# Performance work log

Hardware: AMD Instinct MI355X
Metric: run time of the kernel (lower is better)

The kernel has to match this reference:

```python
import jax, jax.numpy as jnp
import numpy as np

N = 100000      # nodes
E = 1600000     # edges (before self-loops)
DIN = 256
D = 128         # dmid == dout
L = 4           # n_layers
ALPHA = 0.5
THETA = 1.0
EPS = 1e-5      # pyg LayerNorm default eps


def setup_inputs() -> dict:
    key = jax.random.key(0)
    ks = jax.random.split(key, 6)
    x = jax.random.normal(ks[0], (N, DIN), jnp.float32)
    edge_index = jax.random.randint(ks[1], (2, E), 0, N)
    lin1_w = jax.random.normal(ks[2], (D, DIN), jnp.float32) * (1.0 / np.sqrt(DIN))
    lin1_b = jnp.zeros((D,), jnp.float32)
    w1 = jax.random.normal(ks[3], (L, D, D), jnp.float32) * (1.0 / np.sqrt(D))
    w2 = jax.random.normal(ks[4], (L, D, D), jnp.float32) * (1.0 / np.sqrt(D))
    norm_w = jnp.ones((D,), jnp.float32)
    norm_b = jnp.zeros((D,), jnp.float32)
    return {"x": x, "edge_index": edge_index, "lin1_w": lin1_w, "lin1_b": lin1_b,
            "w1": w1, "w2": w2, "norm_w": norm_w, "norm_b": norm_b}


def reference(x, edge_index, lin1_w, lin1_b, w1, w2, norm_w, norm_b):
    # --- gcn_norm: add self-loops, symmetric degree normalization ---
    sl = jnp.arange(N)
    row = jnp.concatenate([edge_index[0], sl])  # sources
    col = jnp.concatenate([edge_index[1], sl])  # targets (aggregation index)
    deg = jax.ops.segment_sum(jnp.ones(row.shape[0], jnp.float32), col, num_segments=N)
    dis = jax.lax.rsqrt(deg)  # deg >= 1 thanks to self-loops
    enorm = dis[row] * dis[col]  # [E+N]

    # --- f_0 = relu(lin1(x)); prev_h = 0 so x_0 arg == f_0 ---
    f0 = jax.nn.relu(x @ lin1_w.T + lin1_b)  # [N, D]
    x0 = ALPHA * f0
    f = f0

    for i in range(L):
        beta = float(np.log(THETA / (i + 1) + 1.0))
        # sparse neighbor aggregation: h = A_hat @ f
        h = jax.ops.segment_sum(f[row] * enorm[:, None], col, num_segments=N)
        h = h * (1.0 - ALPHA)
        # shared_weights=False: two separate identity/weight mixes
        out = ((1.0 - beta) * h + beta * (h @ w1[i])
               + (1.0 - beta) * x0 + beta * (x0 @ w2[i]))
        # pyg LayerNorm mode='graph', batch=None: normalize over all nodes+channels
        m = out.mean()
        s = jnp.sqrt(jnp.mean((out - m) ** 2))
        out = (out - m) / (s + EPS) * norm_w + norm_b
        f = jax.nn.relu(out)

    # dmid == dout -> lin2 is Identity
    return jax.nn.relu(f)
```

## Files before the change

kernel.cpp:

```cpp
#include <hip/hip_runtime.h>
#include <math.h>

constexpr int N    = 100000;
constexpr int E    = 1600000;
constexpr int DIN  = 256;
constexpr int D    = 128;
constexpr int L    = 4;
constexpr float EPS = 1e-5f;
constexpr int NBIN = 256;
constexpr int BINW = 391;
constexpr int SLOT = 8192;

typedef __attribute__((ext_vector_type(8))) short bf16x8;
typedef __attribute__((ext_vector_type(4))) float f32x4;
typedef __attribute__((ext_vector_type(2))) float f32x2;

__device__ inline ushort f2b(float f) {
    uint u = __float_as_uint(f);
    uint r = u + 0x7fffu + ((u >> 16) & 1u);
    return (ushort)(r >> 16);
}
__device__ inline float b2f(ushort b) { return __uint_as_float(((uint)b) << 16); }


__global__ __launch_bounds__(256) void k_countbin(const int* __restrict__ row,
        const int* __restrict__ col, int* __restrict__ cnt, int* __restrict__ bfill,
        int2* __restrict__ stag) {
    __shared__ int hist[NBIN];
    __shared__ int base[NBIN];
    int t = threadIdx.x;
    int e0 = blockIdx.x * 2048 + t * 8;
    if (t < NBIN) hist[t] = 0;
    __syncthreads();
    int r[8], c[8], li[8];
    bool v[8];
    if (e0 + 7 < E) {
        *(int4*)&c[0] = ((const int4*)(col + e0))[0];
        *(int4*)&c[4] = ((const int4*)(col + e0))[1];
        *(int4*)&r[0] = ((const int4*)(row + e0))[0];
        *(int4*)&r[4] = ((const int4*)(row + e0))[1];
        #pragma unroll
        for (int j = 0; j < 8; j++) v[j] = true;
    } else {
        #pragma unroll
        for (int j = 0; j < 8; j++) {
            v[j] = (e0 + j < E);
            if (v[j]) { c[j] = col[e0 + j]; r[j] = row[e0 + j]; }
        }
    }
    #pragma unroll
    for (int j = 0; j < 8; j++) if (v[j]) {
        atomicAdd(&cnt[c[j]], 1);
        li[j] = atomicAdd(&hist[c[j] / BINW], 1);
    }
    __syncthreads();
    if (t < NBIN) base[t] = hist[t] ? atomicAdd(&bfill[t], hist[t]) : 0;
    __syncthreads();
    #pragma unroll
    for (int j = 0; j < 8; j++) if (v[j]) {
        int b = c[j] / BINW;
        stag[(size_t)b * SLOT + base[b] + li[j]] = make_int2(r[j], c[j]);
    }
}

__global__ void k_sumdis(const int* __restrict__ cnt, int* __restrict__ bsum,
                         float* __restrict__ dis) {
    __shared__ int s[256];
    int base = blockIdx.x * 1024;
    int t = threadIdx.x;
    int a = 0;
    for (int j = 0; j < 4; j++) {
        int idx = base + t * 4 + j;
        if (idx < N) {
            int cv = cnt[idx];
            a += cv;
            dis[idx] = rsqrtf((float)cv + 1.0f);
        }
    }
    s[t] = a; __syncthreads();
    for (int off = 128; off > 0; off >>= 1) {
        if (t < off) s[t] += s[t + off];
        __syncthreads();
    }
    if (t == 0) bsum[blockIdx.x] = s[0];
}

__global__ void k_scan(int* __restrict__ bsum, int nb) {
    __shared__ int s[128];
    int t = threadIdx.x;
    int v = (t < nb) ? bsum[t] : 0;
    s[t] = v; __syncthreads();
    for (int off = 1; off < 128; off <<= 1) {
        int x = (t >= off) ? s[t - off] : 0;
        __syncthreads();
        s[t] += x;
        __syncthreads();
    }
    if (t < nb) bsum[t] = s[t] - v;
}

__global__ void k_offsets(const int* __restrict__ cnt, const int* __restrict__ bsum,
                          int* __restrict__ offs, int* __restrict__ cur) {
    __shared__ int ls[256];
    int b = blockIdx.x, t = threadIdx.x;
    int base = b * 1024;
    int v[4]; int s = 0;
    for (int j = 0; j < 4; j++) {
        int idx = base + t * 4 + j;
        v[j] = (idx < N) ? cnt[idx] : 0;
        s += v[j];
    }
    ls[t] = s; __syncthreads();
    for (int off = 1; off < 256; off <<= 1) {
        int x = (t >= off) ? ls[t - off] : 0;
        __syncthreads();
        ls[t] += x;
        __syncthreads();
    }
    int excl = ((t == 0) ? 0 : ls[t - 1]) + bsum[b];
    for (int j = 0; j < 4; j++) {
        int idx = base + t * 4 + j;
        if (idx < N) { offs[idx] = excl; cur[idx] = excl; }
        excl += v[j];
        if (idx == N - 1) offs[N] = excl;
    }
}

__global__ __launch_bounds__(256) void k_unbin(const int2* __restrict__ stag,
        const int* __restrict__ bfill, const float* __restrict__ dis,
        int* __restrict__ cur, int2* __restrict__ csr) {
    int b = blockIdx.x & (NBIN - 1);
    int part = blockIdx.x >> 8;
    int n = bfill[b];
    const int2* sbase = stag + (size_t)b * SLOT;
    for (int i = part * 256 + threadIdx.x; i < n; i += 1024) {
        int2 rc = sbase[i];
        float v = dis[rc.x] * dis[rc.y];
        int pos = atomicAdd(&cur[rc.y], 1);
        csr[pos] = make_int2(rc.x, __float_as_int(v));
    }
}


__global__ void k_prep_w(const float* __restrict__ lin1_w, const float* __restrict__ w1,
                         const float* __restrict__ w2, float4 betas,
                         ushort* __restrict__ wb0, ushort* __restrict__ wbc) {
    int i = blockIdx.x * 256 + threadIdx.x;
    if (i < D * DIN) wb0[i] = f2b(lin1_w[i]);
    if (i < L * D * 256) {
        int l = i >> 15, r = i & 32767, d = r >> 8, k = r & 255;
        float beta = (l == 0) ? betas.x : (l == 1) ? betas.y : (l == 2) ? betas.z : betas.w;
        float v;
        if (k < 128) v = beta * w1[l * 16384 + k * 128 + d] + ((k == d) ? (1.f - beta) : 0.f);
        else { int kk = k - 128; v = beta * w2[l * 16384 + kk * 128 + d] + ((kk == d) ? (1.f - beta) : 0.f); }
        wbc[l * 32768 + d * 256 + k] = f2b(v);
    }
}


__global__ __launch_bounds__(512, 2) void k_f0_mfma(const float* __restrict__ x,
        const ushort* __restrict__ wb, const float* __restrict__ bias,
        ushort* __restrict__ f_bf, ushort* __restrict__ x0_bf) {
    __shared__ uint4 Bl[4096];
    int t = threadIdx.x;
    #pragma unroll
    for (int it = 0; it < 8; it++) {
        int d = it * 512 + t, c = d >> 5, ck = d & 31;
        Bl[c * 32 + (ck ^ (c & 7))] = ((const uint4*)wb)[d];
    }
    __syncthreads();

    int wv = t >> 6, lane = t & 63;
    int l16 = lane & 15, g16 = lane >> 4;
    int row0 = (blockIdx.x * 8 + wv) * 16;
    if (row0 >= N) return;

    const uint4* xb = (const uint4*)(x + (size_t)(row0 + l16) * 256);
    uint4 xr[16];
    #pragma unroll
    for (int ks = 0; ks < 8; ks++) {
        xr[2 * ks]     = xb[ks * 8 + g16 * 2];
        xr[2 * ks + 1] = xb[ks * 8 + g16 * 2 + 1];
    }

    f32x4 acc[8];
    #pragma unroll
    for (int n = 0; n < 8; n++) acc[n] = f32x4{0.f, 0.f, 0.f, 0.f};

    #pragma unroll
    for (int ks = 0; ks < 8; ks++) {
        float4 lo = *(const float4*)&xr[2 * ks];
        float4 hi = *(const float4*)&xr[2 * ks + 1];
        uint4 p;
        p.x = (uint)f2b(lo.x) | ((uint)f2b(lo.y) << 16);
        p.y = (uint)f2b(lo.z) | ((uint)f2b(lo.w) << 16);
        p.z = (uint)f2b(hi.x) | ((uint)f2b(hi.y) << 16);
        p.w = (uint)f2b(hi.z) | ((uint)f2b(hi.w) << 16);
        bf16x8 a = *(bf16x8*)&p;
        int xo = (ks * 4 + g16) ^ (l16 & 7);
        const char* bp = (const char*)Bl + l16 * 512 + xo * 16;
        #pragma unroll
        for (int n = 0; n < 8; n++) {
            bf16x8 b = *(const bf16x8*)(bp + n * 8192);
            acc[n] = __builtin_amdgcn_mfma_f32_16x16x32_bf16(a, b, acc[n], 0, 0, 0);
        }
    }

    float bc[8];
    #pragma unroll
    for (int n = 0; n < 8; n++) bc[n] = bias[n * 16 + l16];
    #pragma unroll
    for (int j = 0; j < 4; j++) {
        int gr = row0 + g16 * 4 + j;
        #pragma unroll
        for (int n = 0; n < 8; n++) {
            float r = fmaxf(acc[n][j] + bc[n], 0.f);
            size_t o = (size_t)gr * 128 + n * 16 + l16;
            f_bf[o] = f2b(r);
            x0_bf[o] = f2b(0.5f * r);
        }
    }
}


__global__ __launch_bounds__(512, 2) void k_combine_mfma(const ushort* __restrict__ g_bf,
        const ushort* __restrict__ x0_bf, const ushort* __restrict__ wb,
        ushort* __restrict__ h_bf, float* __restrict__ sr) {
    __shared__ uint4 Bl[4096];
    __shared__ float red1[512];
    __shared__ float red2[512];
    int t = threadIdx.x;
    #pragma unroll
    for (int it = 0; it < 8; it++) {
        int d = it * 512 + t, c = d >> 5, ck = d & 31;
        Bl[c * 32 + (ck ^ (c & 7))] = ((const uint4*)wb)[d];
    }
    __syncthreads();

    int wv = t >> 6, lane = t & 63;
    int l16 = lane & 15, g16 = lane >> 4;
    int row0 = (blockIdx.x * 8 + wv) * 16;
    bool active = row0 < N;

    f32x4 acc[8];
    #pragma unroll
    for (int n = 0; n < 8; n++) acc[n] = f32x4{0.f, 0.f, 0.f, 0.f};

    if (active) {
        const uint4* ga = (const uint4*)(g_bf  + (size_t)(row0 + l16) * 128);
        const uint4* xa = (const uint4*)(x0_bf + (size_t)(row0 + l16) * 128);
        uint4 ar[8];
        #pragma unroll
        for (int ks = 0; ks < 4; ks++) ar[ks]     = ga[ks * 4 + g16];
        #pragma unroll
        for (int ks = 0; ks < 4; ks++) ar[ks + 4] = xa[ks * 4 + g16];

        #pragma unroll
        for (int ks = 0; ks < 8; ks++) {
            bf16x8 a = *(bf16x8*)&ar[ks];
            int xo = (ks * 4 + g16) ^ (l16 & 7);
            const char* bp = (const char*)Bl + l16 * 512 + xo * 16;
            #pragma unroll
            for (int n = 0; n < 8; n++) {
                bf16x8 b = *(const bf16x8*)(bp + n * 8192);
                acc[n] = __builtin_amdgcn_mfma_f32_16x16x32_bf16(a, b, acc[n], 0, 0, 0);
            }
        }
    }

    float sum = 0.f, sq = 0.f;
    if (active) {
        #pragma unroll
        for (int n = 0; n < 8; n++)
            #pragma unroll
            for (int j = 0; j < 4; j++) { float v = acc[n][j]; sum += v; sq += v * v; }
        #pragma unroll
        for (int j = 0; j < 4; j++) {
            int gr = row0 + g16 * 4 + j;
            #pragma unroll
            for (int n = 0; n < 8; n++)
                h_bf[(size_t)gr * 128 + n * 16 + l16] = f2b(acc[n][j]);
        }
    }

    red1[t] = sum; red2[t] = sq; __syncthreads();
    for (int off = 256; off > 0; off >>= 1) {
        if (t < off) { red1[t] += red1[t + off]; red2[t] += red2[t + off]; }
        __syncthreads();
    }
    if (t == 0) { atomicAdd(&sr[0], red1[0]); atomicAdd(&sr[1], red2[0]); }
}


template <int AFFINE>
__global__ __launch_bounds__(256) void k_agg(const ushort* __restrict__ src,
        const int* __restrict__ offs, const int2* __restrict__ csr,
        const float* __restrict__ dis, const float* __restrict__ sr,
        const float* __restrict__ nw, const float* __restrict__ nb,
        ushort* __restrict__ g_bf) {
    int node = blockIdx.x * 4 + (threadIdx.x >> 6);
    if (node >= N) return;
    int lane = threadIdx.x & 63;
    int q = lane >> 4, cl = lane & 15;
    const uint4* fu = (const uint4*)src;

    f32x2 sc[4], sh[4];
    if constexpr (AFFINE) {
        const float inv_n = 1.0f / ((float)N * (float)D);
        float m = sr[0] * inv_n;
        float var = fmaxf(sr[1] * inv_n - m * m, 0.f);
        float inv = 1.0f / (sqrtf(var) + EPS);
        #pragma unroll
        for (int p = 0; p < 4; p++) {
            float w0 = nw[cl * 8 + 2 * p], w1 = nw[cl * 8 + 2 * p + 1];
            sc[p] = f32x2{inv * w0, inv * w1};
            sh[p] = f32x2{nb[cl * 8 + 2 * p]     - m * inv * w0,
                          nb[cl * 8 + 2 * p + 1] - m * inv * w1};
        }
    }

    f32x2 a2[4];
    #pragma unroll
    for (int p = 0; p < 4; p++) a2[p] = f32x2{0.f, 0.f};

    auto acc8 = [&](float val, uint4 rv) {
        uint uu[4] = {rv.x, rv.y, rv.z, rv.w};
        f32x2 v2 = {val, val};
        #pragma unroll
        for (int p = 0; p < 4; p++) {
            f32x2 c;
            c.x = __uint_as_float(uu[p] << 16);
            c.y = __uint_as_float(uu[p] & 0xffff0000u);
            if constexpr (AFFINE) {
                c = __builtin_elementwise_fma(c, sc[p], sh[p]);
                c = __builtin_elementwise_max(c, f32x2{0.f, 0.f});
            }
            a2[p] = __builtin_elementwise_fma(v2, c, a2[p]);
        }
    };

    float dv = dis[node];
    acc8((q == 0) ? dv * dv : 0.f, fu[(size_t)node * 16 + cl]);

    int end = offs[node + 1];
    int i = offs[node] + q * 4;
    if (i < end) {
        int2 rA[4], rB[4];
        uint4 wA[4];
        #pragma unroll
        for (int s = 0; s < 4; s++) rA[s] = csr[min(i + s, end - 1)];
        #pragma unroll
        for (int s = 0; s < 4; s++) wA[s] = fu[(size_t)rA[s].x * 16 + cl];
        #pragma unroll
        for (int s = 0; s < 4; s++) rB[s] = csr[min(i + 16 + s, end - 1)];
        while (i + 16 < end) {
            uint4 wB[4];
            #pragma unroll
            for (int s = 0; s < 4; s++) wB[s] = fu[(size_t)rB[s].x * 16 + cl];
            int2 rC[4];
            #pragma unroll
            for (int s = 0; s < 4; s++) rC[s] = csr[min(i + 32 + s, end - 1)];
            #pragma unroll
            for (int s = 0; s < 4; s++) acc8(__int_as_float(rA[s].y), wA[s]);
            #pragma unroll
            for (int s = 0; s < 4; s++) { rA[s] = rB[s]; wA[s] = wB[s]; rB[s] = rC[s]; }
            i += 16;
        }
        #pragma unroll
        for (int s = 0; s < 4; s++) {
            float v = (i + s < end) ? __int_as_float(rA[s].y) : 0.f;
            acc8(v, wA[s]);
        }
    }

    #pragma unroll
    for (int p = 0; p < 4; p++) {
        a2[p].x += __shfl_xor(a2[p].x, 16, 64);
        a2[p].x += __shfl_xor(a2[p].x, 32, 64);
        a2[p].y += __shfl_xor(a2[p].y, 16, 64);
        a2[p].y += __shfl_xor(a2[p].y, 32, 64);
    }
    if (q == 0) {
        uint4 o;
        o.x = (uint)f2b(0.5f * a2[0].x) | ((uint)f2b(0.5f * a2[0].y) << 16);
        o.y = (uint)f2b(0.5f * a2[1].x) | ((uint)f2b(0.5f * a2[1].y) << 16);
        o.z = (uint)f2b(0.5f * a2[2].x) | ((uint)f2b(0.5f * a2[2].y) << 16);
        o.w = (uint)f2b(0.5f * a2[3].x) | ((uint)f2b(0.5f * a2[3].y) << 16);
        ((uint4*)g_bf)[(size_t)node * 16 + cl] = o;
    }
}


__global__ void k_ln_final(const ushort* __restrict__ ob, const float* __restrict__ sr,
                           const float* __restrict__ nw, const float* __restrict__ nb,
                           float* __restrict__ fout) {
    int i = blockIdx.x * 256 + threadIdx.x;
    if (i >= N * 16) return;
    const float inv_n = 1.0f / ((float)N * (float)D);
    float m = sr[0] * inv_n;
    float var = fmaxf(sr[1] * inv_n - m * m, 0.f);
    float inv = 1.0f / (sqrtf(var) + EPS);
    uint4 v = ((const uint4*)ob)[i];
    int c = (i & 15) * 8;
    uint vv[4] = {v.x, v.y, v.z, v.w};
    float r[8];
    #pragma unroll
    for (int qd = 0; qd < 4; qd++) {
        float lo = b2f((ushort)(vv[qd] & 0xffff));
        float hi = b2f((ushort)(vv[qd] >> 16));
        r[2 * qd]     = fmaxf((lo - m) * inv * nw[c + 2 * qd]     + nb[c + 2 * qd], 0.f);
        r[2 * qd + 1] = fmaxf((hi - m) * inv * nw[c + 2 * qd + 1] + nb[c + 2 * qd + 1], 0.f);
    }
    float4 o0 = {r[0], r[1], r[2], r[3]};
    float4 o1 = {r[4], r[5], r[6], r[7]};
    ((float4*)fout)[2 * i] = o0;
    ((float4*)fout)[2 * i + 1] = o1;
}


extern "C" void kernel_launch(void* const* d_in, const int* in_sizes, int n_in,
                              void* d_out, int out_size, void* d_ws, size_t ws_size,
                              hipStream_t stream) {
    const float* x      = (const float*)d_in[0];
    const int*   ei     = (const int*)d_in[1];
    const float* lin1_w = (const float*)d_in[2];
    const float* lin1_b = (const float*)d_in[3];
    const float* w1     = (const float*)d_in[4];
    const float* w2     = (const float*)d_in[5];
    const float* nw     = (const float*)d_in[6];
    const float* nb     = (const float*)d_in[7];
    const int* row = ei;
    const int* col = ei + E;
    float* fout = (float*)d_out;

    char* ws = (char*)d_ws;
    size_t off0 = 0;
    auto alloc = [&](size_t bytes) -> char* {
        char* p = ws + off0;
        off0 = (off0 + bytes + 255) & ~(size_t)255;
        return p;
    };
    ushort* f_bf    = (ushort*)alloc((size_t)N * D * 2);
    ushort* x0_bf   = (ushort*)alloc((size_t)N * D * 2);
    ushort* g_bf    = (ushort*)alloc((size_t)N * D * 2);
    ushort* h_bf    = (ushort*)alloc((size_t)N * D * 2);
    float*  dis     = (float*) alloc((size_t)N * 4);
    char*   zblk    = alloc((size_t)N * 4 + NBIN * 4 + 64);
    int*    cnt     = (int*)zblk;
    int*    bfill   = (int*)(zblk + (size_t)N * 4);
    float*  stats   = (float*)(zblk + (size_t)N * 4 + NBIN * 4);
    int*    offs    = (int*)   alloc((size_t)(N + 1) * 4);
    int*    cur     = (int*)   alloc((size_t)N * 4);
    int*    bsum    = (int*)   alloc((size_t)128 * 4);
    int2*   stag    = (int2*)  alloc((size_t)NBIN * SLOT * 8);
    int2*   csr     = (int2*)  alloc((size_t)E * 8);
    ushort* wb0     = (ushort*)alloc((size_t)D * DIN * 2);
    ushort* wbc     = (ushort*)alloc((size_t)L * D * 256 * 2);

    hipMemsetAsync(zblk, 0, (size_t)N * 4 + NBIN * 4 + 64, stream);

    k_countbin<<<(E + 2047) / 2048, 256, 0, stream>>>(row, col, cnt, bfill, stag);
    int nbk = (N + 1023) / 1024;
    k_sumdis<<<nbk, 256, 0, stream>>>(cnt, bsum, dis);
    k_scan<<<1, 128, 0, stream>>>(bsum, nbk);
    k_offsets<<<nbk, 256, 0, stream>>>(cnt, bsum, offs, cur);
    k_unbin<<<NBIN * 4, 256, 0, stream>>>(stag, bfill, dis, cur, csr);

    float4 betas;
    betas.x = logf(1.0f / 1.0f + 1.0f);
    betas.y = logf(1.0f / 2.0f + 1.0f);
    betas.z = logf(1.0f / 3.0f + 1.0f);
    betas.w = logf(1.0f / 4.0f + 1.0f);
    k_prep_w<<<(L * D * 256 + 255) / 256, 256, 0, stream>>>(lin1_w, w1, w2, betas, wb0, wbc);

    int GB = (N / 16 + 7) / 8;
    k_f0_mfma<<<GB, 512, 0, stream>>>(x, wb0, lin1_b, f_bf, x0_bf);

    int AGB = (N + 3) / 4;
    for (int i = 0; i < L; i++) {
        if (i == 0)
            k_agg<0><<<AGB, 256, 0, stream>>>(f_bf, offs, csr, dis, nullptr, nw, nb, g_bf);
        else
            k_agg<1><<<AGB, 256, 0, stream>>>(h_bf, offs, csr, dis, stats + 2 * (i - 1),
                                              nw, nb, g_bf);
        k_combine_mfma<<<GB, 512, 0, stream>>>(g_bf, x0_bf, wbc + (size_t)i * D * 256,
                                               h_bf, stats + 2 * i);
    }
    k_ln_final<<<(N * 16 + 255) / 256, 256, 0, stream>>>(h_bf, stats + 6, nw, nb, fout);
}
```

Before: 570.7 us.

## Merge f0 GEMM, edge binning and weight prep into one role-split launch

Merges three independent kernels (edge count/binning, weight preparation, and the first-layer MFMA GEMM) into a single launch whose blocks pick a role by block index. Even and odd blocks are interleaved between the GEMM and the binning, and the tail blocks convert the combined layer weights. The GEMM blocks now convert lin1_w to bf16 themselves when staging it into shared memory, so the separate wb0 buffer goes away. The aim is to cut launch overhead and let the memory-bound binning overlap with the compute-bound GEMM. In exchange, binning blocks now use 512 threads with 4 edges each and inherit the larger shared-memory and launch-bounds footprint of the GEMM role.

Result: faster. 529.3 us, median of 2 (-7.2%).

```diff
diff --git a/kernel.cpp b/kernel.cpp
--- a/kernel.cpp
+++ b/kernel.cpp
@@ -11,6 +11,10 @@
 constexpr int BINW = 391;
 constexpr int SLOT = 8192;
 
+constexpr int F0B   = 782;
+constexpr int CBB   = 782;
+constexpr int PREPB = 64;
+
 typedef __attribute__((ext_vector_type(8))) short bf16x8;
 typedef __attribute__((ext_vector_type(4))) float f32x4;
 typedef __attribute__((ext_vector_type(2))) float f32x2;
@@ -23,45 +27,133 @@
 __device__ inline float b2f(ushort b) { return __uint_as_float(((uint)b) << 16); }
 
 
-__global__ __launch_bounds__(256) void k_countbin(const int* __restrict__ row,
-        const int* __restrict__ col, int* __restrict__ cnt, int* __restrict__ bfill,
-        int2* __restrict__ stag) {
-    __shared__ int hist[NBIN];
-    __shared__ int base[NBIN];
+__global__ __launch_bounds__(512, 2) void k_f0_countbin(
+        const float* __restrict__ x, const float* __restrict__ lin1_w,
+        const float* __restrict__ bias, ushort* __restrict__ f_bf,
+        ushort* __restrict__ x0_bf,
+        const int* __restrict__ row, const int* __restrict__ col,
+        int* __restrict__ cnt, int* __restrict__ bfill, int2* __restrict__ stag,
+        const float* __restrict__ w1, const float* __restrict__ w2, float4 betas,
+        ushort* __restrict__ wbc) {
+    __shared__ uint4 Bl[4096];
     int t = threadIdx.x;
-    int e0 = blockIdx.x * 2048 + t * 8;
-    if (t < NBIN) hist[t] = 0;
+
+    if (blockIdx.x >= F0B + CBB) {
+        int base = (blockIdx.x - (F0B + CBB)) * 2048 + t * 4;
+        #pragma unroll
+        for (int j = 0; j < 4; j++) {
+            int i = base + j;
+            if (i < L * D * 256) {
+                int l = i >> 15, r = i & 32767, d = r >> 8, k = r & 255;
+                float beta = (l == 0) ? betas.x : (l == 1) ? betas.y
+                           : (l == 2) ? betas.z : betas.w;
+                float v;
+                if (k < 128) v = beta * w1[l * 16384 + k * 128 + d] + ((k == d) ? (1.f - beta) : 0.f);
+                else { int kk = k - 128; v = beta * w2[l * 16384 + kk * 128 + d] + ((kk == d) ? (1.f - beta) : 0.f); }
+                wbc[l * 32768 + d * 256 + k] = f2b(v);
+            }
+        }
+        return;
+    }
+
+    int role = blockIdx.x & 1, rid = blockIdx.x >> 1;
+
+    if (role == 1) {
+        int* hist = (int*)Bl;
+        int* base = hist + NBIN;
+        if (t < NBIN) hist[t] = 0;
+        __syncthreads();
+        int e0 = rid * 2048 + t * 4;
+        bool val = (e0 < E);
+        int r[4], c[4], li[4];
+        if (val) {
+            *(int4*)&c[0] = *(const int4*)(col + e0);
+            *(int4*)&r[0] = *(const int4*)(row + e0);
+            #pragma unroll
+            for (int j = 0; j < 4; j++) {
+                atomicAdd(&cnt[c[j]], 1);
+                li[j] = atomicAdd(&hist[c[j] / BINW], 1);
+            }
+        }
+        __syncthreads();
+        if (t < NBIN) base[t] = hist[t] ? atomicAdd(&bfill[t], hist[t]) : 0;
+        __syncthreads();
+        if (val) {
+            #pragma unroll
+            for (int j = 0; j < 4; j++) {
+                int b = c[j] / BINW;
+                stag[(size_t)b * SLOT + base[b] + li[j]] = make_int2(r[j], c[j]);
+            }
+        }
+        return;
+    }
+
+    #pragma unroll
+    for (int it = 0; it < 8; it++) {
+        int d = it * 512 + t, c = d >> 5, ck = d & 31;
+        const float4* src = (const float4*)(lin1_w + c * 256 + ck * 8);
+        float4 lo = src[0], hi = src[1];
+        uint4 p;
+        p.x = (uint)f2b(lo.x) | ((uint)f2b(lo.y) << 16);
+        p.y = (uint)f2b(lo.z) | ((uint)f2b(lo.w) << 16);
+        p.z = (uint)f2b(hi.x) | ((uint)f2b(hi.y) << 16);
+        p.w = (uint)f2b(hi.z) | ((uint)f2b(hi.w) << 16);
+        Bl[c * 32 + (ck ^ (c & 7))] = p;
+    }
     __syncthreads();
-    int r[8], c[8], li[8];
-    bool v[8];
-    if (e0 + 7 < E) {
-        *(int4*)&c[0] = ((const int4*)(col + e0))[0];
-        *(int4*)&c[4] = ((const int4*)(col + e0))[1];
-        *(int4*)&r[0] = ((const int4*)(row + e0))[0];
-        *(int4*)&r[4] = ((const int4*)(row + e0))[1];
-        #pragma unroll
-        for (int j = 0; j < 8; j++) v[j] = true;
-    } else {
-        #pragma unroll
-        for (int j = 0; j < 8; j++) {
-            v[j] = (e0 + j < E);
-            if (v[j]) { c[j] = col[e0 + j]; r[j] = row[e0 + j]; }
-        }
-    }
-    #pragma unroll
-    for (int j = 0; j < 8; j++) if (v[j]) {
-        atomicAdd(&cnt[c[j]], 1);
-        li[j] = atomicAdd(&hist[c[j] / BINW], 1);
-    }
-    __syncthreads();
-    if (t < NBIN) base[t] = hist[t] ? atomicAdd(&bfill[t], hist[t]) : 0;
-    __syncthreads();
-    #pragma unroll
-    for (int j = 0; j < 8; j++) if (v[j]) {
-        int b = c[j] / BINW;
-        stag[(size_t)b * SLOT + base[b] + li[j]] = make_int2(r[j], c[j]);
-    }
-}
+
+    int wv = t >> 6, lane = t & 63;
+    int l16 = lane & 15, g16 = lane >> 4;
+    int row0 = (rid * 8 + wv) * 16;
+    if (row0 >= N) return;
+
+    const uint4* xb = (const uint4*)(x + (size_t)(row0 + l16) * 256);
+    uint4 xr[16];
+    #pragma unroll
+    for (int ks = 0; ks < 8; ks++) {
+        xr[2 * ks]     = xb[ks * 8 + g16 * 2];
+        xr[2 * ks + 1] = xb[ks * 8 + g16 * 2 + 1];
+    }
+
+    f32x4 acc[8];
+    #pragma unroll
+    for (int n = 0; n < 8; n++) acc[n] = f32x4{0.f, 0.f, 0.f, 0.f};
+
+    #pragma unroll
+    for (int ks = 0; ks < 8; ks++) {
+        float4 lo = *(const float4*)&xr[2 * ks];
+        float4 hi = *(const float4*)&xr[2 * ks + 1];
+        uint4 p;
+        p.x = (uint)f2b(lo.x) | ((uint)f2b(lo.y) << 16);
+        p.y = (uint)f2b(lo.z) | ((uint)f2b(lo.w) << 16);
+        p.z = (uint)f2b(hi.x) | ((uint)f2b(hi.y) << 16);
+        p.w = (uint)f2b(hi.z) | ((uint)f2b(hi.w) << 16);
+        bf16x8 a = *(bf16x8*)&p;
+        int xo = (ks * 4 + g16) ^ (l16 & 7);
+        const char* bp = (const char*)Bl + l16 * 512 + xo * 16;
+        #pragma unroll
+        for (int n = 0; n < 8; n++) {
+            bf16x8 b = *(const bf16x8*)(bp + n * 8192);
+            acc[n] = __builtin_amdgcn_mfma_f32_16x16x32_bf16(a, b, acc[n], 0, 0, 0);
+        }
+    }
+
+    float bc[8];
+    #pragma unroll
+    for (int n = 0; n < 8; n++) bc[n] = bias[n * 16 + l16];
+    #pragma unroll
+    for (int j = 0; j < 4; j++) {
+        int gr = row0 + g16 * 4 + j;
+        #pragma unroll
+        for (int n = 0; n < 8; n++) {
+            float r = fmaxf(acc[n][j] + bc[n], 0.f);
+            size_t o = (size_t)gr * 128 + n * 16 + l16;
+            f_bf[o] = f2b(r);
+            x0_bf[o] = f2b(0.5f * r);
+        }
+    }
+}
+
 
 __global__ void k_sumdis(const int* __restrict__ cnt, int* __restrict__ bsum,
                          float* __restrict__ dis) {
@@ -138,87 +230,6 @@
         float v = dis[rc.x] * dis[rc.y];
         int pos = atomicAdd(&cur[rc.y], 1);
         csr[pos] = make_int2(rc.x, __float_as_int(v));
-    }
-}
-
-
-__global__ void k_prep_w(const float* __restrict__ lin1_w, const float* __restrict__ w1,
-                         const float* __restrict__ w2, float4 betas,
-                         ushort* __restrict__ wb0, ushort* __restrict__ wbc) {
-    int i = blockIdx.x * 256 + threadIdx.x;
-    if (i < D * DIN) wb0[i] = f2b(lin1_w[i]);
-    if (i < L * D * 256) {
-        int l = i >> 15, r = i & 32767, d = r >> 8, k = r & 255;
-        float beta = (l == 0) ? betas.x : (l == 1) ? betas.y : (l == 2) ? betas.z : betas.w;
-        float v;
-        if (k < 128) v = beta * w1[l * 16384 + k * 128 + d] + ((k == d) ? (1.f - beta) : 0.f);
-        else { int kk = k - 128; v = beta * w2[l * 16384 + kk * 128 + d] + ((kk == d) ? (1.f - beta) : 0.f); }
-        wbc[l * 32768 + d * 256 + k] = f2b(v);
-    }
-}
-
-
-__global__ __launch_bounds__(512, 2) void k_f0_mfma(const float* __restrict__ x,
-        const ushort* __restrict__ wb, const float* __restrict__ bias,
-        ushort* __restrict__ f_bf, ushort* __restrict__ x0_bf) {
-    __shared__ uint4 Bl[4096];
-    int t = threadIdx.x;
-    #pragma unroll
-    for (int it = 0; it < 8; it++) {
-        int d = it * 512 + t, c = d >> 5, ck = d & 31;
-        Bl[c * 32 + (ck ^ (c & 7))] = ((const uint4*)wb)[d];
-    }
-    __syncthreads();
-
-    int wv = t >> 6, lane = t & 63;
-    int l16 = lane & 15, g16 = lane >> 4;
-    int row0 = (blockIdx.x * 8 + wv) * 16;
-    if (row0 >= N) return;
-
-    const uint4* xb = (const uint4*)(x + (size_t)(row0 + l16) * 256);
-    uint4 xr[16];
-    #pragma unroll
-    for (int ks = 0; ks < 8; ks++) {
-        xr[2 * ks]     = xb[ks * 8 + g16 * 2];
-        xr[2 * ks + 1] = xb[ks * 8 + g16 * 2 + 1];
-    }
-
-    f32x4 acc[8];
-    #pragma unroll
-    for (int n = 0; n < 8; n++) acc[n] = f32x4{0.f, 0.f, 0.f, 0.f};
-
-    #pragma unroll
-    for (int ks = 0; ks < 8; ks++) {
-        float4 lo = *(const float4*)&xr[2 * ks];
-        float4 hi = *(const float4*)&xr[2 * ks + 1];
-        uint4 p;
-        p.x = (uint)f2b(lo.x) | ((uint)f2b(lo.y) << 16);
-        p.y = (uint)f2b(lo.z) | ((uint)f2b(lo.w) << 16);
-        p.z = (uint)f2b(hi.x) | ((uint)f2b(hi.y) << 16);
-        p.w = (uint)f2b(hi.z) | ((uint)f2b(hi.w) << 16);
-        bf16x8 a = *(bf16x8*)&p;
-        int xo = (ks * 4 + g16) ^ (l16 & 7);
-        const char* bp = (const char*)Bl + l16 * 512 + xo * 16;
-        #pragma unroll
-        for (int n = 0; n < 8; n++) {
-            bf16x8 b = *(const bf16x8*)(bp + n * 8192);
-            acc[n] = __builtin_amdgcn_mfma_f32_16x16x32_bf16(a, b, acc[n], 0, 0, 0);
-        }
-    }
-
-    float bc[8];
-    #pragma unroll
-    for (int n = 0; n < 8; n++) bc[n] = bias[n * 16 + l16];
-    #pragma unroll
-    for (int j = 0; j < 4; j++) {
-        int gr = row0 + g16 * 4 + j;
-        #pragma unroll
-        for (int n = 0; n < 8; n++) {
-            float r = fmaxf(acc[n][j] + bc[n], 0.f);
-            size_t o = (size_t)gr * 128 + n * 16 + l16;
-            f_bf[o] = f2b(r);
-            x0_bf[o] = f2b(0.5f * r);
-        }
     }
 }
 
@@ -454,28 +465,27 @@
     int*    bsum    = (int*)   alloc((size_t)128 * 4);
     int2*   stag    = (int2*)  alloc((size_t)NBIN * SLOT * 8);
     int2*   csr     = (int2*)  alloc((size_t)E * 8);
-    ushort* wb0     = (ushort*)alloc((size_t)D * DIN * 2);
     ushort* wbc     = (ushort*)alloc((size_t)L * D * 256 * 2);
 
     hipMemsetAsync(zblk, 0, (size_t)N * 4 + NBIN * 4 + 64, stream);
 
-    k_countbin<<<(E + 2047) / 2048, 256, 0, stream>>>(row, col, cnt, bfill, stag);
+    float4 betas;
+    betas.x = logf(1.0f / 1.0f + 1.0f);
+    betas.y = logf(1.0f / 2.0f + 1.0f);
+    betas.z = logf(1.0f / 3.0f + 1.0f);
+    betas.w = logf(1.0f / 4.0f + 1.0f);
+
+    k_f0_countbin<<<F0B + CBB + PREPB, 512, 0, stream>>>(
+        x, lin1_w, lin1_b, f_bf, x0_bf, row, col, cnt, bfill, stag,
+        w1, w2, betas, wbc);
+
     int nbk = (N + 1023) / 1024;
     k_sumdis<<<nbk, 256, 0, stream>>>(cnt, bsum, dis);
     k_scan<<<1, 128, 0, stream>>>(bsum, nbk);
     k_offsets<<<nbk, 256, 0, stream>>>(cnt, bsum, offs, cur);
     k_unbin<<<NBIN * 4, 256, 0, stream>>>(stag, bfill, dis, cur, csr);
 
-    float4 betas;
-    betas.x = logf(1.0f / 1.0f + 1.0f);
-    betas.y = logf(1.0f / 2.0f + 1.0f);
-    betas.z = logf(1.0f / 3.0f + 1.0f);
-    betas.w = logf(1.0f / 4.0f + 1.0f);
-    k_prep_w<<<(L * D * 256 + 255) / 256, 256, 0, stream>>>(lin1_w, w1, w2, betas, wb0, wbc);
-
     int GB = (N / 16 + 7) / 8;
-    k_f0_mfma<<<GB, 512, 0, stream>>>(x, wb0, lin1_b, f_bf, x0_bf);
-
     int AGB = (N + 3) / 4;
     for (int i = 0; i < L; i++) {
         if (i == 0)
```
